# Kernel tuning notes

Hardware: AMD Instinct MI355X
Metric: run time of the kernel (lower is better)

## Reference

```python
import jax, jax.numpy as jnp
import numpy as np

N_NODES = 100000
K_HOPS = 2


def _add_self_loops(edge_index, n):
    loop = jnp.arange(n, dtype=edge_index.dtype)
    src = jnp.concatenate([edge_index[0], loop])
    dst = jnp.concatenate([edge_index[1], loop])
    return src, dst


def _gcn_norm(src, dst, n):
    # symmetric normalization D^-1/2 (A+I) D^-1/2
    deg = jax.ops.segment_sum(jnp.ones_like(dst, dtype=jnp.float32), dst, num_segments=n)
    dinv = jnp.where(deg > 0, jax.lax.rsqrt(deg), 0.0)
    return dinv[src] * dinv[dst]  # [E]


def setup_inputs() -> dict:
    key = jax.random.key(0)
    k1, k2, k3, k4, k5 = jax.random.split(key, 5)
    in_f, out_f = 128, 64
    x = jax.random.normal(k1, (N_NODES, in_f), dtype=jnp.float32)
    edge_index = jax.random.randint(k2, (2, 1600000), 0, N_NODES, dtype=jnp.int64)
    s1 = 1.0 / np.sqrt(in_f)
    W1 = jax.random.uniform(k3, (in_f, in_f), dtype=jnp.float32, minval=-s1, maxval=s1)
    b1 = jnp.zeros((in_f,), dtype=jnp.float32)
    W2 = jax.random.uniform(k4, (out_f, in_f), dtype=jnp.float32, minval=-s1, maxval=s1)
    b2 = jnp.zeros((out_f,), dtype=jnp.float32)
    return {"x": x, "edge_index": edge_index, "W1": W1, "b1": b1, "W2": W2, "b2": b2}


def reference(x, edge_index, W1, b1, W2, b2):
    n = x.shape[0]
    src, dst = _add_self_loops(edge_index, n)
    norm = _gcn_norm(src, dst, n)
    for _ in range(K_HOPS):
        msg = x[src] * norm[:, None]                      # [E+N, F] gather
        x = jax.ops.segment_sum(msg, dst, num_segments=n)  # scatter-add
    # transform: Linear -> ReLU -> Linear -> log_softmax
    h = jax.nn.relu(x @ W1.T + b1)
    logits = h @ W2.T + b2
    return jax.nn.log_softmax(logits, axis=1)
```

## Files before the change

kernel.cpp:

```cpp
#include <hip/hip_runtime.h>
#include <math.h>

#define CAP 64
#define NSLICE 64
#define SLMAX 1568
#define QCAP 50000

typedef __attribute__((ext_vector_type(8))) short short8;
typedef __attribute__((ext_vector_type(4))) float f32x4;
typedef __attribute__((ext_vector_type(4))) int int4v;

static __device__ inline unsigned short f2bf(float f) {
    unsigned int u = __float_as_uint(f);
    u += 0x7fffu + ((u >> 16) & 1u);
    return (unsigned short)(u >> 16);
}
static __device__ inline float bf_lo(unsigned int u) { return __uint_as_float(u << 16); }
static __device__ inline float bf_hi(unsigned int u) { return __uint_as_float(u & 0xffff0000u); }
static __device__ inline unsigned int pack2(float lo, float hi) {
    return ((unsigned int)f2bf(hi) << 16) | (unsigned int)f2bf(lo);
}


__global__ __launch_bounds__(256) void part_k(
    const int* __restrict__ dst, const int* __restrict__ src, int E,
    unsigned long long mul, int2* __restrict__ queue, int* __restrict__ qcnt)
{
    __shared__ int lcnt[NSLICE];
    __shared__ int gbase[NSLICE];
    if (threadIdx.x < NSLICE) lcnt[threadIdx.x] = 0;
    __syncthreads();

    int base = blockIdx.x * 2048 + threadIdx.x * 8;
    int nv = E - base; nv = nv > 8 ? 8 : (nv < 0 ? 0 : nv);

    int d[8], sv[8], sl[8], lp[8];
    if (nv == 8) {
        int4v da = __builtin_nontemporal_load((const int4v*)(dst + base));
        int4v db = __builtin_nontemporal_load((const int4v*)(dst + base + 4));
        int4v sa = __builtin_nontemporal_load((const int4v*)(src + base));
        int4v sb = __builtin_nontemporal_load((const int4v*)(src + base + 4));
#pragma unroll
        for (int j = 0; j < 4; j++) {
            d[j] = da[j]; sv[j] = sa[j];
            d[4 + j] = db[j]; sv[4 + j] = sb[j];
        }
    } else {
        for (int j = 0; j < nv; j++) { d[j] = dst[base + j]; sv[j] = src[base + j]; }
    }

#pragma unroll
    for (int j = 0; j < 8; j++) {
        if (j < nv) {
            sl[j] = (int)(((unsigned long long)(unsigned)d[j] * mul) >> 40);
            lp[j] = atomicAdd(&lcnt[sl[j]], 1);
        }
    }
    __syncthreads();
    if (threadIdx.x < NSLICE)
        gbase[threadIdx.x] = atomicAdd(&qcnt[threadIdx.x], lcnt[threadIdx.x]);
    __syncthreads();
#pragma unroll
    for (int j = 0; j < 8; j++) {
        if (j < nv) {
            int p = gbase[sl[j]] + lp[j];
            if (p < QCAP) queue[(size_t)sl[j] * QCAP + p] = make_int2(d[j], sv[j]);
        }
    }
}


__global__ __launch_bounds__(256) void scat_lds_k(
    const int2* __restrict__ queue, const int* __restrict__ qcnt,
    int sl, int n, int* __restrict__ cnt, int* __restrict__ bkt)
{
    int s  = blockIdx.x;
    int lo = s * sl;
    int hi = lo + sl < n ? lo + sl : n;
    int nn = hi - lo;
    if (nn <= 0) return;

    __shared__ int cur[SLMAX];
    for (int i = threadIdx.x; i < nn; i += 256) cur[i] = 0;
    __syncthreads();

    int m = qcnt[s]; if (m > QCAP) m = QCAP;
    const long long* __restrict__ q = (const long long*)(queue + (size_t)s * QCAP);
    for (int i = threadIdx.x; i < m; i += 256) {
        long long r = __builtin_nontemporal_load(q + i);
        int d  = (int)(r & 0xffffffffll);
        int sv = (int)(r >> 32);
        int pos = atomicAdd(&cur[d - lo], 1);
        if (pos < CAP) bkt[(size_t)d * CAP + pos] = sv;
    }
    __syncthreads();
    for (int i = threadIdx.x; i < nn; i += 256) cnt[lo + i] = cur[i];
}

__global__ void dinv_k(const int* __restrict__ cnt, float* __restrict__ dinv, int n) {
    int v = blockIdx.x * blockDim.x + threadIdx.x;
    if (v < n) dinv[v] = rsqrtf((float)(cnt[v] + 1));
}


__global__ void conv_x_k(const float2* __restrict__ x, const float* __restrict__ dinv,
                         unsigned int* __restrict__ xb, int n) {
    int i = blockIdx.x * blockDim.x + threadIdx.x;
    if (i < n * 64) {
        float sc = dinv[i >> 6];
        float2 v = x[i];
        xb[i] = pack2(v.x * sc, v.y * sc);
    }
}

__global__ void conv_w_k(const float2* __restrict__ in, unsigned int* __restrict__ out, int n2) {
    int i = blockIdx.x * blockDim.x + threadIdx.x;
    if (i < n2) {
        float2 v = in[i];
        out[i] = pack2(v.x, v.y);
    }
}


template<bool SQ>
__global__ __launch_bounds__(256) void gather_b_k(
    const unsigned int* __restrict__ xin,
    const int* __restrict__ cnt, const int* __restrict__ bkt,
    const float* __restrict__ dinv,
    unsigned int* __restrict__ xout, int n)
{
    int v = blockIdx.x * 4 + (threadIdx.x >> 6);
    if (v >= n) return;
    int l = threadIdx.x & 63;
    int c = cnt[v]; if (c > CAP) c = CAP;
    const int* __restrict__ b = bkt + (size_t)v * CAP;

    unsigned int us = xin[(size_t)v * 64 + l];
    float ax = 0.f, ay = 0.f;

    for (int i = 0; i < c; i += 8) {
        int4v b0 = *(const int4v*)(b + i);
        int4v b1 = *(const int4v*)(b + i + 4);
        int idx[8];
#pragma unroll
        for (int j = 0; j < 4; j++) idx[j]     = (i + j     < c) ? b0[j] : v;
#pragma unroll
        for (int j = 0; j < 4; j++) idx[4 + j] = (i + 4 + j < c) ? b1[j] : v;
        unsigned int u[8];
#pragma unroll
        for (int j = 0; j < 8; j++) u[j] = xin[(size_t)idx[j] * 64 + l];
#pragma unroll
        for (int j = 0; j < 8; j++) {
            if (i + j < c) { ax += bf_lo(u[j]); ay += bf_hi(u[j]); }
        }
    }

    ax += bf_lo(us);
    ay += bf_hi(us);

    float dv = dinv[v];
    float sc = SQ ? dv * dv : dv;
    xout[(size_t)v * 64 + l] = pack2(ax * sc, ay * sc);
}

__global__ __launch_bounds__(256) void transform_mfma_k(
    const unsigned short* __restrict__ x2b,
    const unsigned short* __restrict__ w1b,
    const float* __restrict__ b1,
    const unsigned short* __restrict__ w2b,
    const float* __restrict__ b2,
    float* __restrict__ out, int n)
{
    __shared__ __align__(16) unsigned short Hs[64][152];

    int t = threadIdx.x;
    int w = t >> 6;
    int l = t & 63;
    int lg = l >> 4;
    int ll = l & 15;
    int node0 = blockIdx.x * 64;

    int nrow = node0 + w * 16 + ll;
    int crow = nrow < n ? nrow : (n - 1);
    const unsigned short* xrow = x2b + (size_t)crow * 128 + lg * 8;
    short8 a[4];
#pragma unroll
    for (int kb = 0; kb < 4; kb++)
        a[kb] = *(const short8*)(xrow + kb * 32);

    f32x4 acc[8];
#pragma unroll
    for (int nt = 0; nt < 8; nt++) {
        float bv = b1[nt * 16 + ll];
        acc[nt][0] = bv; acc[nt][1] = bv; acc[nt][2] = bv; acc[nt][3] = bv;
    }
#pragma unroll
    for (int nt = 0; nt < 8; nt++) {
        const unsigned short* wrow = w1b + (size_t)(nt * 16 + ll) * 128 + lg * 8;
#pragma unroll
        for (int kb = 0; kb < 4; kb++) {
            short8 bf = *(const short8*)(wrow + kb * 32);
            acc[nt] = __builtin_amdgcn_mfma_f32_16x16x32_bf16(a[kb], bf, acc[nt], 0, 0, 0);
        }
    }

#pragma unroll
    for (int nt = 0; nt < 8; nt++) {
#pragma unroll
        for (int r = 0; r < 4; r++) {
            float hv = fmaxf(acc[nt][r], 0.f);
            Hs[w * 16 + lg * 4 + r][nt * 16 + ll] = f2bf(hv);
        }
    }

    short8 ha[4];
#pragma unroll
    for (int kb = 0; kb < 4; kb++)
        ha[kb] = *(const short8*)&Hs[w * 16 + ll][kb * 32 + lg * 8];

    f32x4 acc2[4];
#pragma unroll
    for (int nt = 0; nt < 4; nt++) {
        float bv = b2[nt * 16 + ll];
        acc2[nt][0] = bv; acc2[nt][1] = bv; acc2[nt][2] = bv; acc2[nt][3] = bv;
        const unsigned short* wrow = w2b + (size_t)(nt * 16 + ll) * 128 + lg * 8;
#pragma unroll
        for (int kb = 0; kb < 4; kb++) {
            short8 bf = *(const short8*)(wrow + kb * 32);
            acc2[nt] = __builtin_amdgcn_mfma_f32_16x16x32_bf16(ha[kb], bf, acc2[nt], 0, 0, 0);
        }
    }

#pragma unroll
    for (int r = 0; r < 4; r++) {
        float m = fmaxf(fmaxf(acc2[0][r], acc2[1][r]), fmaxf(acc2[2][r], acc2[3][r]));
        m = fmaxf(m, __shfl_xor(m, 1));
        m = fmaxf(m, __shfl_xor(m, 2));
        m = fmaxf(m, __shfl_xor(m, 4));
        m = fmaxf(m, __shfl_xor(m, 8));
        float s = __expf(acc2[0][r] - m) + __expf(acc2[1][r] - m) +
                  __expf(acc2[2][r] - m) + __expf(acc2[3][r] - m);
        s += __shfl_xor(s, 1);
        s += __shfl_xor(s, 2);
        s += __shfl_xor(s, 4);
        s += __shfl_xor(s, 8);
        float lse = m + __logf(s);
        int node = node0 + w * 16 + lg * 4 + r;
        if (node < n) {
#pragma unroll
            for (int nt = 0; nt < 4; nt++)
                out[(size_t)node * 64 + nt * 16 + ll] = acc2[nt][r] - lse;
        }
    }
}


static inline size_t align256(size_t x) { return (x + 255) & ~(size_t)255; }

extern "C" void kernel_launch(void* const* d_in, const int* in_sizes, int n_in,
                              void* d_out, int out_size, void* d_ws, size_t ws_size,
                              hipStream_t stream) {
    const float* x  = (const float*)d_in[0];
    const int*   ei = (const int*)d_in[1];
    const float* W1 = (const float*)d_in[2];
    const float* b1 = (const float*)d_in[3];
    const float* W2 = (const float*)d_in[4];
    const float* b2 = (const float*)d_in[5];
    float* out = (float*)d_out;

    int n = in_sizes[0] / 128;
    int E = in_sizes[1] / 2;
    const int* src = ei;
    const int* dst = ei + E;

    char* w = (char*)d_ws;
    size_t off = 0;
    int*          cnt  = (int*)(w + off);          off += align256((size_t)n * sizeof(int));
    int*          qcnt = (int*)(w + off);          off += 256;
    float*        dinv = (float*)(w + off);        off += align256((size_t)n * sizeof(float));
    int*          bkt  = (int*)(w + off);          off += align256((size_t)n * CAP * sizeof(int));
    unsigned int* xb   = (unsigned int*)(w + off); off += align256((size_t)n * 64 * sizeof(unsigned int));
    unsigned int* z1b  = (unsigned int*)(w + off); off += align256((size_t)n * 64 * sizeof(unsigned int));
    unsigned int* x2b  = (unsigned int*)(w + off); off += align256((size_t)n * 64 * sizeof(unsigned int));
    unsigned int* w1b  = (unsigned int*)(w + off); off += align256((size_t)128 * 64 * sizeof(unsigned int));
    unsigned int* w2b  = (unsigned int*)(w + off);
    int2* queue = (int2*)xb;

    int tb = 256;
    int gb_n = (n + tb - 1) / tb;
    int gb_x = (n * 64 + tb - 1) / tb;
    int gb_g = (n + 3) / 4;
    int gb_p = (E + 2047) / 2048;

    int sl = (n + NSLICE - 1) / NSLICE;
    unsigned long long mul = ((1ULL << 40) + (unsigned long long)sl - 1) / (unsigned long long)sl;

    (void)hipMemsetAsync(qcnt, 0, 256, stream);
    part_k<<<gb_p, tb, 0, stream>>>(dst, src, E, mul, queue, qcnt);
    scat_lds_k<<<NSLICE, tb, 0, stream>>>(queue, qcnt, sl, n, cnt, bkt);
    dinv_k<<<gb_n, tb, 0, stream>>>(cnt, dinv, n);

    conv_x_k<<<gb_x, tb, 0, stream>>>((const float2*)x, dinv, xb, n);
    conv_w_k<<<(128 * 64 + tb - 1) / tb, tb, 0, stream>>>((const float2*)W1, w1b, 128 * 64);
    conv_w_k<<<(64 * 64 + tb - 1) / tb, tb, 0, stream>>>((const float2*)W2, w2b, 64 * 64);

    gather_b_k<true ><<<gb_g, tb, 0, stream>>>(xb,  cnt, bkt, dinv, z1b, n);
    gather_b_k<false><<<gb_g, tb, 0, stream>>>(z1b, cnt, bkt, dinv, x2b, n);

    transform_mfma_k<<<(n + 63) / 64, 256, 0, stream>>>(
        (const unsigned short*)x2b, (const unsigned short*)w1b, b1,
        (const unsigned short*)w2b, b2, out, n);
}
```

Before: 267.8 us.

## Fuse dinv into scatter, merge weight converts, readlane neighbor indices, more slices

Several independent changes. The degree-normalization kernel is folded into the LDS scatter kernel, and the two weight-conversion launches become one, which removes launches. The slice count is doubled, with the queue capacity per slice halved, so the scatter step runs on more blocks. The gather kernel now loads one bucket entry per lane and broadcasts each neighbor index with readlane, rather than doing vector loads of the bucket plus predicated padding. This trades redundant index loads and masked work for scalar broadcasts, at the risk of queue overflow if a slice receives more than its halved capacity.

```diff
diff --git a/kernel.cpp b/kernel.cpp
--- a/kernel.cpp
+++ b/kernel.cpp
@@ -2,9 +2,9 @@
 #include <math.h>
 
 #define CAP 64
-#define NSLICE 64
-#define SLMAX 1568
-#define QCAP 50000
+#define NSLICE 128
+#define SLMAX 784
+#define QCAP 25000
 
 typedef __attribute__((ext_vector_type(8))) short short8;
 typedef __attribute__((ext_vector_type(4))) float f32x4;
@@ -72,7 +72,8 @@
 
 __global__ __launch_bounds__(256) void scat_lds_k(
     const int2* __restrict__ queue, const int* __restrict__ qcnt,
-    int sl, int n, int* __restrict__ cnt, int* __restrict__ bkt)
+    int sl, int n, int* __restrict__ cnt, float* __restrict__ dinv,
+    int* __restrict__ bkt)
 {
     int s  = blockIdx.x;
     int lo = s * sl;
@@ -94,12 +95,11 @@
         if (pos < CAP) bkt[(size_t)d * CAP + pos] = sv;
     }
     __syncthreads();
-    for (int i = threadIdx.x; i < nn; i += 256) cnt[lo + i] = cur[i];
-}
-
-__global__ void dinv_k(const int* __restrict__ cnt, float* __restrict__ dinv, int n) {
-    int v = blockIdx.x * blockDim.x + threadIdx.x;
-    if (v < n) dinv[v] = rsqrtf((float)(cnt[v] + 1));
+    for (int i = threadIdx.x; i < nn; i += 256) {
+        int c = cur[i];
+        cnt[lo + i] = c;
+        dinv[lo + i] = rsqrtf((float)(c + 1));
+    }
 }
 
 
@@ -113,11 +113,15 @@
     }
 }
 
-__global__ void conv_w_k(const float2* __restrict__ in, unsigned int* __restrict__ out, int n2) {
+__global__ void conv_w2_k(const float2* __restrict__ w1, unsigned int* __restrict__ o1, int n1,
+                          const float2* __restrict__ w2, unsigned int* __restrict__ o2, int n2) {
     int i = blockIdx.x * blockDim.x + threadIdx.x;
-    if (i < n2) {
-        float2 v = in[i];
-        out[i] = pack2(v.x, v.y);
+    if (i < n1) {
+        float2 v = w1[i];
+        o1[i] = pack2(v.x, v.y);
+    } else if (i < n1 + n2) {
+        float2 v = w2[i - n1];
+        o2[i - n1] = pack2(v.x, v.y);
     }
 }
 
@@ -133,26 +137,36 @@
     if (v >= n) return;
     int l = threadIdx.x & 63;
     int c = cnt[v]; if (c > CAP) c = CAP;
-    const int* __restrict__ b = bkt + (size_t)v * CAP;
-
+
+    int be = bkt[(size_t)v * CAP + l];
     unsigned int us = xin[(size_t)v * 64 + l];
     float ax = 0.f, ay = 0.f;
 
-    for (int i = 0; i < c; i += 8) {
-        int4v b0 = *(const int4v*)(b + i);
-        int4v b1 = *(const int4v*)(b + i + 4);
-        int idx[8];
-#pragma unroll
-        for (int j = 0; j < 4; j++) idx[j]     = (i + j     < c) ? b0[j] : v;
-#pragma unroll
-        for (int j = 0; j < 4; j++) idx[4 + j] = (i + 4 + j < c) ? b1[j] : v;
+    int i = 0;
+    for (; i + 8 <= c; i += 8) {
         unsigned int u[8];
 #pragma unroll
-        for (int j = 0; j < 8; j++) u[j] = xin[(size_t)idx[j] * 64 + l];
-#pragma unroll
         for (int j = 0; j < 8; j++) {
-            if (i + j < c) { ax += bf_lo(u[j]); ay += bf_hi(u[j]); }
-        }
+            int s = __builtin_amdgcn_readlane(be, i + j);
+            u[j] = xin[(size_t)s * 64 + l];
+        }
+#pragma unroll
+        for (int j = 0; j < 8; j++) { ax += bf_lo(u[j]); ay += bf_hi(u[j]); }
+    }
+    for (; i + 4 <= c; i += 4) {
+        unsigned int u[4];
+#pragma unroll
+        for (int j = 0; j < 4; j++) {
+            int s = __builtin_amdgcn_readlane(be, i + j);
+            u[j] = xin[(size_t)s * 64 + l];
+        }
+#pragma unroll
+        for (int j = 0; j < 4; j++) { ax += bf_lo(u[j]); ay += bf_hi(u[j]); }
+    }
+    for (; i < c; i++) {
+        int s = __builtin_amdgcn_readlane(be, i);
+        unsigned int u = xin[(size_t)s * 64 + l];
+        ax += bf_lo(u); ay += bf_hi(u);
     }
 
     ax += bf_lo(us);
@@ -276,7 +290,7 @@
     char* w = (char*)d_ws;
     size_t off = 0;
     int*          cnt  = (int*)(w + off);          off += align256((size_t)n * sizeof(int));
-    int*          qcnt = (int*)(w + off);          off += 256;
+    int*          qcnt = (int*)(w + off);          off += align256(NSLICE * sizeof(int));
     float*        dinv = (float*)(w + off);        off += align256((size_t)n * sizeof(float));
     int*          bkt  = (int*)(w + off);          off += align256((size_t)n * CAP * sizeof(int));
     unsigned int* xb   = (unsigned int*)(w + off); off += align256((size_t)n * 64 * sizeof(unsigned int));
@@ -287,7 +301,6 @@
     int2* queue = (int2*)xb;
 
     int tb = 256;
-    int gb_n = (n + tb - 1) / tb;
     int gb_x = (n * 64 + tb - 1) / tb;
     int gb_g = (n + 3) / 4;
     int gb_p = (E + 2047) / 2048;
@@ -295,14 +308,14 @@
     int sl = (n + NSLICE - 1) / NSLICE;
     unsigned long long mul = ((1ULL << 40) + (unsigned long long)sl - 1) / (unsigned long long)sl;
 
-    (void)hipMemsetAsync(qcnt, 0, 256, stream);
+    (void)hipMemsetAsync(qcnt, 0, NSLICE * sizeof(int), stream);
     part_k<<<gb_p, tb, 0, stream>>>(dst, src, E, mul, queue, qcnt);
-    scat_lds_k<<<NSLICE, tb, 0, stream>>>(queue, qcnt, sl, n, cnt, bkt);
-    dinv_k<<<gb_n, tb, 0, stream>>>(cnt, dinv, n);
+    scat_lds_k<<<NSLICE, tb, 0, stream>>>(queue, qcnt, sl, n, cnt, dinv, bkt);
 
     conv_x_k<<<gb_x, tb, 0, stream>>>((const float2*)x, dinv, xb, n);
-    conv_w_k<<<(128 * 64 + tb - 1) / tb, tb, 0, stream>>>((const float2*)W1, w1b, 128 * 64);
-    conv_w_k<<<(64 * 64 + tb - 1) / tb, tb, 0, stream>>>((const float2*)W2, w2b, 64 * 64);
+    int n1 = 128 * 64, n2 = 64 * 64;
+    conv_w2_k<<<(n1 + n2 + tb - 1) / tb, tb, 0, stream>>>(
+        (const float2*)W1, w1b, n1, (const float2*)W2, w2b, n2);
 
     gather_b_k<true ><<<gb_g, tb, 0, stream>>>(xb,  cnt, bkt, dinv, z1b, n);
     gather_b_k<false><<<gb_g, tb, 0, stream>>>(z1b, cnt, bkt, dinv, x2b, n);
```

Result: faster. 242.1 us (-9.6%).
